# Optimization experiments

Hardware: AMD Instinct MI355X
Metric: run time of the kernel (lower is better)

The kernel has to match this reference:

```python
import jax, jax.numpy as jnp
import numpy as np

C = 256
CQ = C // 8  # query/key channels


def setup_inputs() -> dict:
    key = jax.random.key(0)
    ks = jax.random.split(key, 8)
    B, H, W = 4, 64, 64
    x = jax.random.normal(ks[0], (B, C, H, W), dtype=jnp.float32)
    mask = jax.random.uniform(ks[1], (B, 1, H, W), dtype=jnp.float32)
    # 1x1 conv weights stored as [out_ch, in_ch] (kernel_size=1)
    s = 1.0 / np.sqrt(C)
    Wq = jax.random.uniform(ks[2], (CQ, C), dtype=jnp.float32, minval=-s, maxval=s)
    bq = jax.random.uniform(ks[3], (CQ,), dtype=jnp.float32, minval=-s, maxval=s)
    Wk = jax.random.uniform(ks[4], (CQ, C), dtype=jnp.float32, minval=-s, maxval=s)
    bk = jax.random.uniform(ks[5], (CQ,), dtype=jnp.float32, minval=-s, maxval=s)
    Wv = jax.random.uniform(ks[6], (C, C), dtype=jnp.float32, minval=-s, maxval=s)
    bv = jax.random.uniform(ks[7], (C,), dtype=jnp.float32, minval=-s, maxval=s)
    gamma = jnp.ones((1,), dtype=jnp.float32)
    return {"x": x, "mask": mask, "Wq": Wq, "bq": bq, "Wk": Wk, "bk": bk,
            "Wv": Wv, "bv": bv, "gamma": gamma}


def reference(x, mask, Wq, bq, Wk, bk, Wv, bv, gamma):
    B, Cc, H, W = x.shape
    N = H * W
    xf = x.reshape(B, Cc, N)                  # [B, C, N]
    m = mask.reshape(B, 1, N)                 # [B, 1, N]
    # 1x1 convs == per-pixel linear maps over channels
    q = jnp.einsum('oc,bcn->bon', Wq, xf) + bq[None, :, None]  # [B, CQ, N]
    k = jnp.einsum('oc,bcn->bon', Wk, xf) + bk[None, :, None]  # [B, CQ, N]
    v = jnp.einsum('oc,bcn->bon', Wv, xf) + bv[None, :, None]  # [B, C,  N]
    q = q * m
    k = k * m
    energy = jnp.einsum('bci,bcj->bij', q, k)  # [B, N, N] (queries x keys)
    attn = jax.nn.softmax(energy, axis=-1)
    out = jnp.einsum('bcj,bij->bci', v, attn)  # [B, C, N]
    out = out.reshape(B, Cc, H, W)
    return gamma * out + x
```

## Files before the change

### kernel.cpp

```cpp
#include <hip/hip_runtime.h>
#include <math.h>

#define CC 256
#define NPIX 4096
#define BATCH 4
#define LOG2E 1.4426950408889634f

typedef __attribute__((ext_vector_type(8)))  short short8;
typedef __attribute__((ext_vector_type(8)))  int   int32x8;
typedef __attribute__((ext_vector_type(16))) float f32x16;

union FragU { short8 v; short s[8]; unsigned u[4]; uint2 d[2]; };
union V8  { uint4 q[2]; int32x8 iv; };
union B8  { unsigned u[8]; int32x8 iv; };

__device__ inline unsigned pkbf(float a, float b) {
    unsigned x = __float_as_uint(a), y = __float_as_uint(b);
    x = (x + 0x7FFFu + ((x >> 16) & 1u)) >> 16;
    y = (y + 0x7FFFu + ((y >> 16) & 1u)) & 0xFFFF0000u;
    return x | y;
}
__device__ inline unsigned short bf1(float a) {
    unsigned x = __float_as_uint(a);
    return (unsigned short)((x + 0x7FFFu + ((x >> 16) & 1u)) >> 16);
}
__device__ inline float ex2(float x) { return __builtin_amdgcn_exp2f(x); }
__device__ inline unsigned pk4fp8(float a, float b, float c, float d) {
    int r = __builtin_amdgcn_cvt_pk_fp8_f32(a, b, 0, false);
    r = __builtin_amdgcn_cvt_pk_fp8_f32(c, d, r, true);
    return (unsigned)r;
}
__device__ inline f32x16 zero16() {
    f32x16 v;
    #pragma unroll
    for (int i = 0; i < 16; ++i) v[i] = 0.0f;
    return v;
}
__device__ inline f32x16 mfma32(short8 a, short8 b, f32x16 c) {
    return __builtin_amdgcn_mfma_f32_32x32x16_bf16(a, b, c, 0, 0, 0);
}
__device__ inline f32x16 mfma64s(int32x8 a, int32x8 b, f32x16 c) {
    return __builtin_amdgcn_mfma_scale_f32_32x32x64_f8f6f4(
        a, b, c, 0 , 0 , 0, 0x7F, 0, 0x7F);
}

__global__ __launch_bounds__(256, 2) void prep_kernel(
    const float* __restrict__ x,
    const float* __restrict__ Wq, const float* __restrict__ Wk,
    const float* __restrict__ Wv,
    unsigned short* __restrict__ xT, unsigned short* __restrict__ Wfrag)
{
    const int t = threadIdx.x;
    const int bid = blockIdx.x;
    if (bid < 256) {
        __shared__ unsigned short xs[256 * 68];
        const int b = bid >> 6, u = bid & 63;
        const int p0 = u * 64;
        const float* xb = x + (size_t)b * CC * NPIX + p0;
        #pragma unroll
        for (int k = 0; k < 16; ++k) {
            int c = (t >> 4) + 16 * k;
            int p4 = (t & 15) * 4;
            int p4s = p4 ^ (((c >> 3) & 15) << 2);
            float4 v = *(const float4*)(xb + (size_t)c * NPIX + p4);
            *(uint2*)&xs[c * 68 + p4s] = make_uint2(pkbf(v.x, v.y), pkbf(v.z, v.w));
        }
        __syncthreads();
        const int w = t >> 6, l = t & 63;
        const int c8 = l & 31;
        const int psw = ((c8 & 15) << 2);
        #pragma unroll
        for (int i = 0; i < 8; ++i) {
            int p = i * 8 + w * 2 + (l >> 5);
            int ps = p ^ psw;
            unsigned short tmp[8];
            #pragma unroll
            for (int j = 0; j < 8; ++j) tmp[j] = xs[(c8 * 8 + j) * 68 + ps];
            uint4 o;
            o.x = tmp[0] | ((unsigned)tmp[1] << 16);
            o.y = tmp[2] | ((unsigned)tmp[3] << 16);
            o.z = tmp[4] | ((unsigned)tmp[5] << 16);
            o.w = tmp[6] | ((unsigned)tmp[7] << 16);
            *(uint4*)(xT + (size_t)(b * NPIX + p0 + p) * 256 + c8 * 8) = o;
        }
    } else {
        const int wb = bid - 256;
        const int l = t & 63, rr = t >> 6;
        #pragma unroll
        for (int e = 0; e < 4; ++e) {
            int gs = wb * 4 + e;
            int g = gs >> 4, s = gs & 15;
            const float* src; float scale = 1.0f; int oc0 = 0;
            if (g == 0)      { src = Wq; scale = LOG2E; }
            else if (g == 1) { src = Wk; }
            else             { src = Wv; oc0 = (g - 2) * 32; }
            int row = oc0 + (l & 31);
            int kb2 = 16 * s + 8 * (l >> 5) + rr * 2;
            float v0 = src[(size_t)row * CC + kb2] * scale;
            float v1 = src[(size_t)row * CC + kb2 + 1] * scale;
            *(unsigned*)(Wfrag + (size_t)(gs * 64 + l) * 8 + rr * 2) = pkbf(v0, v1);
        }
    }
}

__global__ __launch_bounds__(320, 3) void proj_mfma(
    const unsigned short* __restrict__ xT, const unsigned short* __restrict__ Wfrag,
    const float* __restrict__ mask,
    const float* __restrict__ bq, const float* __restrict__ bk,
    const float* __restrict__ bv,
    unsigned short* __restrict__ qT, unsigned short* __restrict__ kT,
    unsigned char* __restrict__ vI)
{
    __shared__ unsigned short xls[64 * 260];
    const int t = threadIdx.x;
    const int w = t >> 6, l = t & 63, L = l & 31, h = l >> 5;
    const int bid = blockIdx.x;
    const int b    = (bid >> 1) & 3;
    const int u    = ((bid >> 3) << 1) | (bid & 1);
    const int p0   = (u >> 1) * 64;
    const int half = u & 1;
    const int ocg  = half * 5 + w;

    const unsigned short* xg = xT + (size_t)(b * NPIX + p0) * 256;
    #pragma unroll
    for (int r = 0; r < 7; ++r) {
        int idx = r * 2560 + t * 8;
        if (idx < 16384) {
            uint4 d = *(const uint4*)(xg + idx);
            int p = idx >> 8, c = idx & 255;
            *(uint2*)&xls[p * 260 + c]     = make_uint2(d.x, d.y);
            *(uint2*)&xls[p * 260 + c + 4] = make_uint2(d.z, d.w);
        }
    }

    FragU wf[16];
    const unsigned short* wp = Wfrag + (size_t)(ocg * 16 * 64 + l) * 8;
    #pragma unroll
    for (int s = 0; s < 16; ++s) wf[s].v = *(const short8*)(wp + s * 512);

    float bcol;
    if (ocg == 0)      bcol = bq[L] * LOG2E;
    else if (ocg == 1) bcol = bk[L];
    else               bcol = bv[(ocg - 2) * 32 + L];
    const float* mb = mask + (size_t)b * NPIX;
    __syncthreads();

    #pragma unroll
    for (int mt = 0; mt < 2; ++mt) {
        const int pp = 32 * mt;
        f32x16 acc = zero16();
        #pragma unroll
        for (int s = 0; s < 16; ++s) {
            FragU af;
            const unsigned short* ap = &xls[(pp + L) * 260 + 16 * s + 8 * h];
            af.d[0] = *(const uint2*)(ap);
            af.d[1] = *(const uint2*)(ap + 4);
            acc = mfma32(af.v, wf[s].v, acc);
        }
        if (ocg < 2) {
            unsigned short* dst = (ocg ? kT : qT) + (size_t)b * NPIX * 32;
            #pragma unroll
            for (int r = 0; r < 16; ++r) {
                int prow = (r & 3) + 8 * (r >> 2) + 4 * h;
                float mv = mb[p0 + pp + prow];
                dst[(size_t)(p0 + pp + prow) * 32 + L] = bf1((acc[r] + bcol) * mv);
            }
        } else {
            const int cg = ocg - 2;
            const int jb32 = p0 + pp;
            unsigned char* dst = vI + (size_t)b * (1 << 20)
                + (size_t)(jb32 >> 6) * 16384 + cg * 2048
                + (((jb32 >> 5) & 1) * 32 + L) * 32 + 4 * h;
            #pragma unroll
            for (int m = 0; m < 4; ++m) {
                unsigned pk = pk4fp8(acc[4*m]   + bcol, acc[4*m+1] + bcol,
                                     acc[4*m+2] + bcol, acc[4*m+3] + bcol);
                *(unsigned*)(dst + 8 * m) = pk;
            }
        }
    }
}

__global__ __launch_bounds__(256, 2) void attn_mfma(
    const unsigned short* __restrict__ qT, const unsigned short* __restrict__ kT,
    const unsigned char* __restrict__ vI, const float* __restrict__ x,
    const float* __restrict__ gamma, float* __restrict__ out)
{
    __shared__ float mls[2][4][32];
    __shared__ float obuf[4][2048];

    const int t = threadIdx.x;
    const int w = t >> 6, l = t & 63, L = l & 31, h = l >> 5;
    const int bid = blockIdx.x;
    const int b  = (bid >> 1) & 3;
    const int it = (bid >> 3) * 2 + (bid & 1);
    const int i0 = it * 32;

    const unsigned short* qrow = qT + ((size_t)b * NPIX + i0 + L) * 32 + 8 * h;
    short8 qf0 = *(const short8*)(qrow);
    short8 qf1 = *(const short8*)(qrow + 16);

    const int jbase = w * 1024;
    const unsigned char* kp = (const unsigned char*)kT
        + (size_t)b * NPIX * 64 + (size_t)jbase * 64 + (size_t)L * 64 + 16 * h;
    short8 ka0 = *(const short8*)(kp);
    short8 ka1 = *(const short8*)(kp + 32);
    short8 kb0 = *(const short8*)(kp + 2048);
    short8 kb1 = *(const short8*)(kp + 2080);
    kp += 4096;
    const unsigned char* vp = vI + (size_t)b * (1 << 20)
        + (size_t)(jbase >> 6) * 16384 + (size_t)l * 32;

    f32x16 acc[8];
    #pragma unroll
    for (int cg = 0; cg < 8; ++cg) acc[cg] = zero16();
    float m_run = -INFINITY, l_run = 0.0f;
    bool warm = false;

    for (int itr = 0; itr < 16; ++itr) {
        f32x16 s0 = zero16(), s1 = zero16();
        __builtin_amdgcn_s_setprio(1);
        s0 = mfma32(ka0, qf0, s0);
        s0 = mfma32(ka1, qf1, s0);
        s1 = mfma32(kb0, qf0, s1);
        s1 = mfma32(kb1, qf1, s1);
        __builtin_amdgcn_s_setprio(0);

        ka0 = *(const short8*)(kp);
        ka1 = *(const short8*)(kp + 32);
        kb0 = *(const short8*)(kp + 2048);
        kb1 = *(const short8*)(kp + 2080);
        kp += 4096;

        V8 vv[4];
        #pragma unroll
        for (int cg = 0; cg < 4; ++cg) {
            vv[cg].q[0] = *(const uint4*)(vp + cg * 2048);
            vv[cg].q[1] = *(const uint4*)(vp + cg * 2048 + 16);
        }

        float t0 = fmaxf(fmaxf(s0[0],  s0[4]),  s0[8]);
        float t1 = fmaxf(fmaxf(s0[1],  s0[5]),  s0[9]);
        float t2 = fmaxf(fmaxf(s0[2],  s0[6]),  s0[10]);
        float t3 = fmaxf(fmaxf(s0[3],  s0[7]),  s0[11]);
        t0 = fmaxf(fmaxf(t0, s0[12]), s1[0]);
        t1 = fmaxf(fmaxf(t1, s0[13]), s1[1]);
        t2 = fmaxf(fmaxf(t2, s0[14]), s1[2]);
        t3 = fmaxf(fmaxf(t3, s0[15]), s1[3]);
        t0 = fmaxf(fmaxf(t0, s1[4]),  s1[8]);
        t1 = fmaxf(fmaxf(t1, s1[5]),  s1[9]);
        t2 = fmaxf(fmaxf(t2, s1[6]),  s1[10]);
        t3 = fmaxf(fmaxf(t3, s1[7]),  s1[11]);
        t0 = fmaxf(t0, s1[12]);
        t1 = fmaxf(t1, s1[13]);
        t2 = fmaxf(t2, s1[14]);
        t3 = fmaxf(t3, s1[15]);
        float tmax = fmaxf(fmaxf(fmaxf(t0, t1), t2), t3);
        tmax = fmaxf(tmax, __shfl_xor(tmax, 32));

        if (__ballot(tmax > m_run + 3.0f)) {
            float m_new = fmaxf(m_run, tmax);
            if (warm) {
                float alpha = ex2(m_run - m_new);
                l_run *= alpha;
                #pragma unroll
                for (int cg = 0; cg < 8; ++cg)
                    #pragma unroll
                    for (int r = 0; r < 16; ++r) acc[cg][r] *= alpha;
            }
            m_run = m_new;
            warm = true;
        }

        float z0 = 0, z1 = 0, z2 = 0, z3 = 0;
        #pragma unroll
        for (int r = 0; r < 16; r += 4) {
            s0[r]   = ex2(s0[r]   - m_run); z0 += s0[r];
            s0[r+1] = ex2(s0[r+1] - m_run); z1 += s0[r+1];
            s0[r+2] = ex2(s0[r+2] - m_run); z2 += s0[r+2];
            s0[r+3] = ex2(s0[r+3] - m_run); z3 += s0[r+3];
        }
        #pragma unroll
        for (int r = 0; r < 16; r += 4) {
            s1[r]   = ex2(s1[r]   - m_run); z0 += s1[r];
            s1[r+1] = ex2(s1[r+1] - m_run); z1 += s1[r+1];
            s1[r+2] = ex2(s1[r+2] - m_run); z2 += s1[r+2];
            s1[r+3] = ex2(s1[r+3] - m_run); z3 += s1[r+3];
        }
        float ssum = (z0 + z1) + (z2 + z3);
        ssum += __shfl_xor(ssum, 32);
        l_run += ssum;

        unsigned u0[4], u1[4], p0[4], p1[4];
        #pragma unroll
        for (int m = 0; m < 4; ++m) {
            u0[m] = pk4fp8(s0[4*m], s0[4*m+1], s0[4*m+2], s0[4*m+3]);
            u1[m] = pk4fp8(s1[4*m], s1[4*m+1], s1[4*m+2], s1[4*m+3]);
        }
        #pragma unroll
        for (int q = 0; q < 4; ++q) {
            p0[q] = (unsigned)__shfl_xor((int)u0[q], 32);
            p1[q] = (unsigned)__shfl_xor((int)u1[q], 32);
        }
        B8 bf;
        #pragma unroll
        for (int m = 0; m < 4; ++m) {
            unsigned oh = h ? u1[m] : u0[m];
            unsigned ph = h ? p1[m] : p0[m];
            bf.u[2*m]     = h ? ph : oh;
            bf.u[2*m + 1] = h ? oh : ph;
        }

        __builtin_amdgcn_s_setprio(1);
        #pragma unroll
        for (int cg = 0; cg < 4; ++cg) acc[cg] = mfma64s(vv[cg].iv, bf.iv, acc[cg]);
        #pragma unroll
        for (int cg = 0; cg < 4; ++cg) {
            vv[cg].q[0] = *(const uint4*)(vp + (cg + 4) * 2048);
            vv[cg].q[1] = *(const uint4*)(vp + (cg + 4) * 2048 + 16);
        }
        #pragma unroll
        for (int cg = 0; cg < 4; ++cg) acc[cg + 4] = mfma64s(vv[cg].iv, bf.iv, acc[cg + 4]);
        __builtin_amdgcn_s_setprio(0);
        vp += 16384;
    }

    if (h == 0) { mls[0][w][L] = m_run; mls[1][w][L] = l_run; }
    __syncthreads();
    float m0 = mls[0][0][L], m1 = mls[0][1][L], m2 = mls[0][2][L], m3 = mls[0][3][L];
    float ms = fmaxf(fmaxf(fmaxf(m0, m1), m2), m3);
    float f0 = ex2(m0 - ms), f1 = ex2(m1 - ms);
    float f2 = ex2(m2 - ms), f3 = ex2(m3 - ms);
    float lstar = f0 * mls[1][0][L] + f1 * mls[1][1][L]
                + f2 * mls[1][2][L] + f3 * mls[1][3][L];
    const float scale = gamma[0] / lstar;
    const float g0 = scale * f0, g1 = scale * f1;
    const float g2 = scale * f2, g3 = scale * f3;

    const int ti = t & 31, trow = t >> 5;
    for (int ck = 0; ck < 4; ++ck) {
        #pragma unroll
        for (int half = 0; half < 2; ++half) {
            #pragma unroll
            for (int r = 0; r < 16; ++r) {
                int prow = (r & 3) + 8 * (r >> 2) + 4 * h;
                obuf[w][half * 1024 + prow * 32 + L] = acc[2 * ck + half][r];
            }
        }
        __syncthreads();
        #pragma unroll
        for (int rr = 0; rr < 8; ++rr) {
            int cr = trow + 8 * rr;
            int idx = cr * 32 + ti;
            float sum = g0 * obuf[0][idx] + g1 * obuf[1][idx]
                      + g2 * obuf[2][idx] + g3 * obuf[3][idx];
            size_t gi = ((size_t)b * CC + ck * 64 + cr) * NPIX + i0 + ti;
            out[gi] = sum + x[gi];
        }
        __syncthreads();
    }
}

extern "C" void kernel_launch(void* const* d_in, const int* in_sizes, int n_in,
                              void* d_out, int out_size, void* d_ws, size_t ws_size,
                              hipStream_t stream) {
    const float* x     = (const float*)d_in[0];
    const float* mask  = (const float*)d_in[1];
    const float* Wq    = (const float*)d_in[2];
    const float* bq    = (const float*)d_in[3];
    const float* Wk    = (const float*)d_in[4];
    const float* bk    = (const float*)d_in[5];
    const float* Wv    = (const float*)d_in[6];
    const float* bv    = (const float*)d_in[7];
    const float* gamma = (const float*)d_in[8];
    float* out = (float*)d_out;

    unsigned short* ws = (unsigned short*)d_ws;
    unsigned short* qT = ws;
    unsigned short* kT = qT + (size_t)BATCH * NPIX * 32;
    unsigned char*  vI = (unsigned char*)(kT + (size_t)BATCH * NPIX * 32);
    unsigned short* xT = (unsigned short*)(vI + (size_t)BATCH * CC * NPIX);
    unsigned short* Wfrag = xT + (size_t)BATCH * NPIX * 256;

    prep_kernel<<<296, 256, 0, stream>>>(x, Wq, Wk, Wv, xT, Wfrag);
    proj_mfma<<<512, 320, 0, stream>>>(xT, Wfrag, mask, bq, bk, bv, qT, kT, vI);
    attn_mfma<<<512, 256, 0, stream>>>(qT, kT, vI, x, gamma, out);
}
```

Baseline: 128.5 us.

## Fuse x transpose and bf16 conversion into projection kernel, drop xT buffer

The projection kernel now reads fp32 x directly, converts it to bf16 and transposes it into shared memory, instead of reading a pre-transposed bf16 xT produced by a separate prep pass. The weight-fragment prep becomes a small standalone kernel. Each projection block now covers 64 pixels for all 10 output-channel groups, using 640 threads in 256 blocks. This removes the global write and re-read of the 8 MB xT intermediate. In exchange, x is now read with strided fp32 loads and written to shared memory in a scattered pattern that may cause bank conflicts, and the larger blocks change occupancy.

```diff
diff --git a/kernel.cpp b/kernel.cpp
--- a/kernel.cpp
+++ b/kernel.cpp
@@ -44,67 +44,31 @@
         a, b, c, 0 , 0 , 0, 0x7F, 0, 0x7F);
 }
 
-__global__ __launch_bounds__(256, 2) void prep_kernel(
-    const float* __restrict__ x,
+__global__ __launch_bounds__(256, 2) void prep_w(
     const float* __restrict__ Wq, const float* __restrict__ Wk,
-    const float* __restrict__ Wv,
-    unsigned short* __restrict__ xT, unsigned short* __restrict__ Wfrag)
+    const float* __restrict__ Wv, unsigned short* __restrict__ Wfrag)
 {
     const int t = threadIdx.x;
-    const int bid = blockIdx.x;
-    if (bid < 256) {
-        __shared__ unsigned short xs[256 * 68];
-        const int b = bid >> 6, u = bid & 63;
-        const int p0 = u * 64;
-        const float* xb = x + (size_t)b * CC * NPIX + p0;
-        #pragma unroll
-        for (int k = 0; k < 16; ++k) {
-            int c = (t >> 4) + 16 * k;
-            int p4 = (t & 15) * 4;
-            int p4s = p4 ^ (((c >> 3) & 15) << 2);
-            float4 v = *(const float4*)(xb + (size_t)c * NPIX + p4);
-            *(uint2*)&xs[c * 68 + p4s] = make_uint2(pkbf(v.x, v.y), pkbf(v.z, v.w));
-        }
-        __syncthreads();
-        const int w = t >> 6, l = t & 63;
-        const int c8 = l & 31;
-        const int psw = ((c8 & 15) << 2);
-        #pragma unroll
-        for (int i = 0; i < 8; ++i) {
-            int p = i * 8 + w * 2 + (l >> 5);
-            int ps = p ^ psw;
-            unsigned short tmp[8];
-            #pragma unroll
-            for (int j = 0; j < 8; ++j) tmp[j] = xs[(c8 * 8 + j) * 68 + ps];
-            uint4 o;
-            o.x = tmp[0] | ((unsigned)tmp[1] << 16);
-            o.y = tmp[2] | ((unsigned)tmp[3] << 16);
-            o.z = tmp[4] | ((unsigned)tmp[5] << 16);
-            o.w = tmp[6] | ((unsigned)tmp[7] << 16);
-            *(uint4*)(xT + (size_t)(b * NPIX + p0 + p) * 256 + c8 * 8) = o;
-        }
-    } else {
-        const int wb = bid - 256;
-        const int l = t & 63, rr = t >> 6;
-        #pragma unroll
-        for (int e = 0; e < 4; ++e) {
-            int gs = wb * 4 + e;
-            int g = gs >> 4, s = gs & 15;
-            const float* src; float scale = 1.0f; int oc0 = 0;
-            if (g == 0)      { src = Wq; scale = LOG2E; }
-            else if (g == 1) { src = Wk; }
-            else             { src = Wv; oc0 = (g - 2) * 32; }
-            int row = oc0 + (l & 31);
-            int kb2 = 16 * s + 8 * (l >> 5) + rr * 2;
-            float v0 = src[(size_t)row * CC + kb2] * scale;
-            float v1 = src[(size_t)row * CC + kb2 + 1] * scale;
-            *(unsigned*)(Wfrag + (size_t)(gs * 64 + l) * 8 + rr * 2) = pkbf(v0, v1);
-        }
-    }
-}
-
-__global__ __launch_bounds__(320, 3) void proj_mfma(
-    const unsigned short* __restrict__ xT, const unsigned short* __restrict__ Wfrag,
+    const int wb = blockIdx.x;
+    const int l = t & 63, rr = t >> 6;
+    #pragma unroll
+    for (int e = 0; e < 4; ++e) {
+        int gs = wb * 4 + e;
+        int g = gs >> 4, s = gs & 15;
+        const float* src; float scale = 1.0f; int oc0 = 0;
+        if (g == 0)      { src = Wq; scale = LOG2E; }
+        else if (g == 1) { src = Wk; }
+        else             { src = Wv; oc0 = (g - 2) * 32; }
+        int row = oc0 + (l & 31);
+        int kb2 = 16 * s + 8 * (l >> 5) + rr * 2;
+        float v0 = src[(size_t)row * CC + kb2] * scale;
+        float v1 = src[(size_t)row * CC + kb2 + 1] * scale;
+        *(unsigned*)(Wfrag + (size_t)(gs * 64 + l) * 8 + rr * 2) = pkbf(v0, v1);
+    }
+}
+
+__global__ __launch_bounds__(640, 2) void proj_mfma(
+    const float* __restrict__ x, const unsigned short* __restrict__ Wfrag,
     const float* __restrict__ mask,
     const float* __restrict__ bq, const float* __restrict__ bk,
     const float* __restrict__ bv,
@@ -117,19 +81,22 @@
     const int bid = blockIdx.x;
     const int b    = (bid >> 1) & 3;
     const int u    = ((bid >> 3) << 1) | (bid & 1);
-    const int p0   = (u >> 1) * 64;
-    const int half = u & 1;
-    const int ocg  = half * 5 + w;
-
-    const unsigned short* xg = xT + (size_t)(b * NPIX + p0) * 256;
-    #pragma unroll
-    for (int r = 0; r < 7; ++r) {
-        int idx = r * 2560 + t * 8;
-        if (idx < 16384) {
-            uint4 d = *(const uint4*)(xg + idx);
-            int p = idx >> 8, c = idx & 255;
-            *(uint2*)&xls[p * 260 + c]     = make_uint2(d.x, d.y);
-            *(uint2*)&xls[p * 260 + c + 4] = make_uint2(d.z, d.w);
+    const int p0   = u * 64;
+    const int ocg  = w;
+
+    if (t < 512) {
+        const int pg = t & 15;
+        const int cb = (t >> 4) * 2;
+        const float* xb = x + (size_t)b * CC * NPIX + p0 + pg * 4;
+        #pragma unroll
+        for (int k = 0; k < 4; ++k) {
+            int c = cb + 64 * k;
+            float4 v0 = *(const float4*)(xb + (size_t)c * NPIX);
+            float4 v1 = *(const float4*)(xb + (size_t)(c + 1) * NPIX);
+            *(unsigned*)&xls[(pg * 4 + 0) * 260 + c] = pkbf(v0.x, v1.x);
+            *(unsigned*)&xls[(pg * 4 + 1) * 260 + c] = pkbf(v0.y, v1.y);
+            *(unsigned*)&xls[(pg * 4 + 2) * 260 + c] = pkbf(v0.z, v1.z);
+            *(unsigned*)&xls[(pg * 4 + 3) * 260 + c] = pkbf(v0.w, v1.w);
         }
     }
 
@@ -379,10 +346,10 @@
     unsigned short* qT = ws;
     unsigned short* kT = qT + (size_t)BATCH * NPIX * 32;
     unsigned char*  vI = (unsigned char*)(kT + (size_t)BATCH * NPIX * 32);
-    unsigned short* xT = (unsigned short*)(vI + (size_t)BATCH * CC * NPIX);
-    unsigned short* Wfrag = xT + (size_t)BATCH * NPIX * 256;
-
-    prep_kernel<<<296, 256, 0, stream>>>(x, Wq, Wk, Wv, xT, Wfrag);
-    proj_mfma<<<512, 320, 0, stream>>>(xT, Wfrag, mask, bq, bk, bv, qT, kT, vI);
+    unsigned short* xpad = (unsigned short*)(vI + (size_t)BATCH * CC * NPIX);
+    unsigned short* Wfrag = xpad + (size_t)BATCH * NPIX * 256;
+
+    prep_w<<<40, 256, 0, stream>>>(Wq, Wk, Wv, Wfrag);
+    proj_mfma<<<256, 640, 0, stream>>>(x, Wfrag, mask, bq, bk, bv, qT, kT, vI);
     attn_mfma<<<512, 256, 0, stream>>>(qT, kT, vI, x, gamma, out);
 }
```

Result: faster. 125.2 us (-2.6%).
